# Kernel tuning notes

Measured on AMD Instinct MI355X. Metric: run time of the kernel, lower is better.

The kernel has to match this reference:

```python
import jax, jax.numpy as jnp
import numpy as np

B, S, D, H = 8, 1024, 768, 12
DK = D // H  # 64
EPS = 1e-8


def setup_inputs() -> dict:
    key = jax.random.key(0)
    ks = jax.random.split(key, 12)
    scale = 0.02
    inp = {
        "query": jax.random.normal(ks[0], (B, S, D), jnp.float32),
        "key": jax.random.normal(ks[1], (B, S, D), jnp.float32),
        "value": jax.random.normal(ks[2], (B, S, D), jnp.float32),
        "attention_mask": jnp.ones((B, 1, 1, S), jnp.float32),
        "Wq": jax.random.normal(ks[3], (D, D), jnp.float32) * scale,
        "bq": jnp.zeros((D,), jnp.float32),
        "Wk": jax.random.normal(ks[4], (D, D), jnp.float32) * scale,
        "bk": jnp.zeros((D,), jnp.float32),
        "Wv": jax.random.normal(ks[5], (D, D), jnp.float32) * scale,
        "bv": jnp.zeros((D,), jnp.float32),
        "Wo": jax.random.normal(ks[6], (D, D), jnp.float32) * scale,
        "bo": jnp.zeros((D,), jnp.float32),
        "gamma": jnp.ones((D,), jnp.float32),
        "beta": jnp.zeros((D,), jnp.float32),
    }
    return inp


def _split_heads(x):
    # [B,S,D] -> [B,H,S,DK]
    return x.reshape(B, S, H, DK).transpose(0, 2, 1, 3)


def reference(query, key, value, attention_mask, Wq, bq, Wk, bk, Wv, bv, Wo, bo, gamma, beta):
    origin = query
    q = _split_heads(query @ Wq + bq)
    k = _split_heads(key @ Wk + bk)
    v = _split_heads(value @ Wv + bv)
    # scaled dot-product attention, full [B,H,S,S] score as in original
    score = jnp.einsum('bhqd,bhkd->bhqk', q, k) / jnp.sqrt(jnp.float32(DK))
    score = score + (1.0 - attention_mask) * -10000.0
    attn = jax.nn.softmax(score, axis=-1)
    ctx = jnp.einsum('bhqk,bhkd->bhqd', attn, v)  # [B,H,S,DK]
    ctx = ctx.transpose(0, 2, 1, 3).reshape(B, S, D)
    out = ctx @ Wo + bo
    # residual + LayerNorm
    x = out + origin
    mu = jnp.mean(x, axis=-1, keepdims=True)
    var = jnp.mean(jnp.square(x - mu), axis=-1, keepdims=True)
    out = (x - mu) * jax.lax.rsqrt(var + EPS) * gamma + beta
    return out, attn
```

## Files before the change

### kernel.cpp

```cpp
#include <hip/hip_runtime.h>
#include <cstdint>

typedef unsigned short u16;
typedef __attribute__((ext_vector_type(8))) short bf16x8;
typedef __attribute__((ext_vector_type(4))) float f32x4;
typedef __attribute__((ext_vector_type(8))) unsigned short u16x8;

constexpr int NB = 8;
constexpr int SEQ = 1024;
constexpr int NH = 12;
constexpr int DM = 768;
constexpr int DH = 64;

__device__ __forceinline__ u16 f2bf(float f) {
  unsigned int x = __builtin_bit_cast(unsigned int, f);
  x += 0x7fffu + ((x >> 16) & 1u);
  return (u16)(x >> 16);
}

typedef __attribute__((address_space(1))) void* as1vp;
typedef __attribute__((address_space(3))) void* as3vp;

__device__ __forceinline__ void load_lds16(const u16* g, u16* l) {
  __builtin_amdgcn_global_load_lds((as1vp)(g), (as3vp)(l), 16, 0, 0);
}

template<int TM, int TN, int EPI>
__global__ __launch_bounds__(256)
void gemm_bt(const u16* __restrict__ A, int lda, long long strideA,
             const u16* __restrict__ BT, int ldb, long long strideBT,
             const float* __restrict__ bias,
             const float* __restrict__ extra,
             void* __restrict__ outp,
             int K)
{
  constexpr int BK = 32;
  constexpr int WM = TM / 2, WN = TN / 2;
  constexpr int FM = WM / 16, FN = WN / 16;
  __shared__ u16 As[TM * BK];
  __shared__ u16 Bs[TN * BK];
  const int tid = threadIdx.x;
  const int w = tid >> 6, l = tid & 63;
  const int z = blockIdx.z;
  const u16* Az = A + (long long)z * strideA;
  const u16* Bz = BT + (long long)z * strideBT;
  const int m0 = blockIdx.x * TM, n0 = blockIdx.y * TN;
  const int wm = (w & 1) * WM, wn = (w >> 1) * WN;
  const int quad = l >> 4, md = l & 15;

  f32x4 acc[FM][FN];
  f32x4 zero = {0.f, 0.f, 0.f, 0.f};
  #pragma unroll
  for (int i = 0; i < FM; ++i)
    #pragma unroll
    for (int j = 0; j < FN; ++j) acc[i][j] = zero;

  for (int k0 = 0; k0 < K; k0 += BK) {
    __syncthreads();
    #pragma unroll
    for (int r = 0; r < TM / 64; ++r) {
      int lin = r * 256 + tid;
      int row = lin >> 2, ch = lin & 3;
      load_lds16(Az + (long long)(m0 + row) * lda + k0 + ch * 8, &As[lin * 8]);
    }
    #pragma unroll
    for (int r = 0; r < TN / 64; ++r) {
      int lin = r * 256 + tid;
      int row = lin >> 2, ch = lin & 3;
      load_lds16(Bz + (long long)(n0 + row) * ldb + k0 + ch * 8, &Bs[lin * 8]);
    }
    __syncthreads();
    bf16x8 af[FM], bfr[FN];
    #pragma unroll
    for (int i = 0; i < FM; ++i)
      af[i] = *(const bf16x8*)&As[(wm + i * 16 + md) * BK + quad * 8];
    #pragma unroll
    for (int j = 0; j < FN; ++j)
      bfr[j] = *(const bf16x8*)&Bs[(wn + j * 16 + md) * BK + quad * 8];
    #pragma unroll
    for (int i = 0; i < FM; ++i)
      #pragma unroll
      for (int j = 0; j < FN; ++j)
        acc[i][j] = __builtin_amdgcn_mfma_f32_16x16x32_bf16(af[i], bfr[j], acc[i][j], 0, 0, 0);
  }

  #pragma unroll
  for (int i = 0; i < FM; ++i) {
    #pragma unroll
    for (int j = 0; j < FN; ++j) {
      #pragma unroll
      for (int r = 0; r < 4; ++r) {
        int grow = m0 + wm + i * 16 + quad * 4 + r;
        int gcol = n0 + wn + j * 16 + md;
        float v = acc[i][j][r];
        float vv = v + bias[gcol] + extra[(long long)grow * DM + gcol];
        ((float*)outp)[(long long)grow * DM + gcol] = vv;
      }
    }
  }
}

__global__ __launch_bounds__(256)
void gemm_qkv(const u16* __restrict__ Abase, const u16* __restrict__ Wbase,
              const float* __restrict__ bq, const float* __restrict__ bk,
              const float* __restrict__ bv, u16* __restrict__ outbase)
{
  constexpr int TM = 128, TN = 128, BK = 32;
  constexpr int WM = 64, WN = 64, FM = 4, FN = 4;
  __shared__ u16 As[TM * BK];
  __shared__ u16 Bs[TN * BK];
  const int tid = threadIdx.x;
  const int w = tid >> 6, l = tid & 63;
  const int z = blockIdx.z;
  const long long TOKDM = (long long)NB * SEQ * DM;
  const u16* Az = Abase + (long long)z * TOKDM;
  const u16* Bz = Wbase + (long long)z * DM * DM;
  const float* bias = z == 0 ? bq : z == 1 ? bk : bv;
  u16* o = outbase + (long long)z * TOKDM;
  const int m0 = blockIdx.x * TM, n0 = blockIdx.y * TN;
  const int wm = (w & 1) * WM, wn = (w >> 1) * WN;
  const int quad = l >> 4, md = l & 15;

  f32x4 acc[FM][FN];
  f32x4 zero = {0.f, 0.f, 0.f, 0.f};
  #pragma unroll
  for (int i = 0; i < FM; ++i)
    #pragma unroll
    for (int j = 0; j < FN; ++j) acc[i][j] = zero;

  for (int k0 = 0; k0 < DM; k0 += BK) {
    __syncthreads();
    #pragma unroll
    for (int r = 0; r < 2; ++r) {
      int lin = r * 256 + tid;
      int row = lin >> 2, ch = lin & 3;
      load_lds16(Az + (long long)(m0 + row) * DM + k0 + ch * 8, &As[lin * 8]);
    }
    #pragma unroll
    for (int r = 0; r < 2; ++r) {
      int lin = r * 256 + tid;
      int row = lin >> 2, ch = lin & 3;
      load_lds16(Bz + (long long)(n0 + row) * DM + k0 + ch * 8, &Bs[lin * 8]);
    }
    __syncthreads();
    bf16x8 af[FM], bfr[FN];
    #pragma unroll
    for (int i = 0; i < FM; ++i)
      af[i] = *(const bf16x8*)&As[(wm + i * 16 + md) * BK + quad * 8];
    #pragma unroll
    for (int j = 0; j < FN; ++j)
      bfr[j] = *(const bf16x8*)&Bs[(wn + j * 16 + md) * BK + quad * 8];
    #pragma unroll
    for (int i = 0; i < FM; ++i)
      #pragma unroll
      for (int j = 0; j < FN; ++j)
        acc[i][j] = __builtin_amdgcn_mfma_f32_16x16x32_bf16(af[i], bfr[j], acc[i][j], 0, 0, 0);
  }

  #pragma unroll
  for (int i = 0; i < FM; ++i) {
    #pragma unroll
    for (int j = 0; j < FN; ++j) {
      #pragma unroll
      for (int r = 0; r < 4; ++r) {
        int grow = m0 + wm + i * 16 + quad * 4 + r;
        int gcol = n0 + wn + j * 16 + md;
        int bb = grow >> 10, s = grow & (SEQ - 1);
        int h = gcol >> 6, dk = gcol & (DH - 1);
        float vb = acc[i][j][r] + bias[gcol];
        if (z < 2)
          o[(((long long)(bb * NH + h)) * SEQ + s) * DH + dk] = f2bf(vb);
        else
          o[(((long long)(bb * NH + h)) * DH + dk) * SEQ + s] = f2bf(vb);
      }
    }
  }
}

__global__ __launch_bounds__(256, 2)
void attn_fused(const u16* __restrict__ Qh, const u16* __restrict__ Kh,
                const u16* __restrict__ VT, const float* __restrict__ mask,
                float* __restrict__ attn, u16* __restrict__ ctx)
{
  __shared__ u16 Plds[4 * 32 * 128];
  const int tid = threadIdx.x;
  const int w = tid >> 6, l = tid & 63;
  const int quad = l >> 4, md = l & 15;
  const int dsp = blockIdx.x;
  const int L = (dsp & 7) * 96 + (dsp >> 3);
  const int bh = L >> 3, rb = L & 7;
  const int b = bh / NH, h = bh - b * NH;
  const int m0 = rb * 128;
  const int wm = w * 32;

  const u16* Qb = Qh + (long long)bh * SEQ * DH;
  const u16* Kb = Kh + (long long)bh * SEQ * DH;
  const u16* Vb = VT + (long long)bh * DH * SEQ;
  const float* mrow = mask + b * SEQ;
  float* arow = attn + (long long)bh * SEQ * SEQ;

  bf16x8 aq[2][2];
  #pragma unroll
  for (int i = 0; i < 2; ++i)
    #pragma unroll
    for (int kk = 0; kk < 2; ++kk)
      aq[i][kk] = *(const bf16x8*)(Qb + (long long)(m0 + wm + i * 16 + md) * DH + kk * 32 + quad * 8);

  float m_run[2][4], s_run[2][4];
  #pragma unroll
  for (int i = 0; i < 2; ++i)
    #pragma unroll
    for (int r = 0; r < 4; ++r) { m_run[i][r] = -3.0e38f; s_run[i][r] = 0.0f; }

  f32x4 zero = {0.f, 0.f, 0.f, 0.f};

  for (int t = 0; t < 8; ++t) {
    const int n0 = t * 128;
    float madd[8];
    #pragma unroll
    for (int j = 0; j < 8; ++j)
      madd[j] = (1.0f - mrow[n0 + j * 16 + md]) * -10000.0f;
    f32x4 acc[2][8];
    #pragma unroll
    for (int i = 0; i < 2; ++i)
      #pragma unroll
      for (int j = 0; j < 8; ++j) acc[i][j] = zero;
    #pragma unroll
    for (int j = 0; j < 8; ++j) {
      const u16* kp = Kb + (long long)(n0 + j * 16 + md) * DH + quad * 8;
      bf16x8 b0 = *(const bf16x8*)kp;
      bf16x8 b1 = *(const bf16x8*)(kp + 32);
      #pragma unroll
      for (int i = 0; i < 2; ++i) {
        acc[i][j] = __builtin_amdgcn_mfma_f32_16x16x32_bf16(aq[i][0], b0, acc[i][j], 0, 0, 0);
        acc[i][j] = __builtin_amdgcn_mfma_f32_16x16x32_bf16(aq[i][1], b1, acc[i][j], 0, 0, 0);
      }
    }
    #pragma unroll
    for (int i = 0; i < 2; ++i) {
      #pragma unroll
      for (int r = 0; r < 4; ++r) {
        float sc[8];
        float tm = -3.0e38f;
        #pragma unroll
        for (int j = 0; j < 8; ++j) {
          sc[j] = acc[i][j][r] * 0.125f + madd[j];
          tm = fmaxf(tm, sc[j]);
        }
        #pragma unroll
        for (int s = 1; s < 16; s <<= 1) tm = fmaxf(tm, __shfl_xor(tm, s, 64));
        float mn = fmaxf(m_run[i][r], tm);
        float ps = 0.0f;
        #pragma unroll
        for (int j = 0; j < 8; ++j) ps += __expf(sc[j] - mn);
        #pragma unroll
        for (int s = 1; s < 16; s <<= 1) ps += __shfl_xor(ps, s, 64);
        s_run[i][r] = s_run[i][r] * __expf(m_run[i][r] - mn) + ps;
        m_run[i][r] = mn;
      }
    }
  }
  float inv_s[2][4];
  #pragma unroll
  for (int i = 0; i < 2; ++i)
    #pragma unroll
    for (int r = 0; r < 4; ++r) inv_s[i][r] = 1.0f / s_run[i][r];

  f32x4 cacc[2][4];
  #pragma unroll
  for (int i = 0; i < 2; ++i)
    #pragma unroll
    for (int jd = 0; jd < 4; ++jd) cacc[i][jd] = zero;
  char* Pw = (char*)Plds + w * 8192;

  for (int t = 0; t < 8; ++t) {
    const int n0 = t * 128;
    float madd[8];
    #pragma unroll
    for (int j = 0; j < 8; ++j)
      madd[j] = (1.0f - mrow[n0 + j * 16 + md]) * -10000.0f;
    f32x4 acc[2][8];
    #pragma unroll
    for (int i = 0; i < 2; ++i)
      #pragma unroll
      for (int j = 0; j < 8; ++j) acc[i][j] = zero;
    #pragma unroll
    for (int j = 0; j < 8; ++j) {
      const u16* kp = Kb + (long long)(n0 + j * 16 + md) * DH + quad * 8;
      bf16x8 b0 = *(const bf16x8*)kp;
      bf16x8 b1 = *(const bf16x8*)(kp + 32);
      #pragma unroll
      for (int i = 0; i < 2; ++i) {
        acc[i][j] = __builtin_amdgcn_mfma_f32_16x16x32_bf16(aq[i][0], b0, acc[i][j], 0, 0, 0);
        acc[i][j] = __builtin_amdgcn_mfma_f32_16x16x32_bf16(aq[i][1], b1, acc[i][j], 0, 0, 0);
      }
    }
    #pragma unroll
    for (int i = 0; i < 2; ++i) {
      #pragma unroll
      for (int j = 0; j < 8; ++j) {
        #pragma unroll
        for (int r = 0; r < 4; ++r) {
          float p = __expf(acc[i][j][r] * 0.125f + madd[j] - m_run[i][r]) * inv_s[i][r];
          int grow = m0 + wm + i * 16 + quad * 4 + r;
          __builtin_nontemporal_store(p, &arow[(long long)grow * SEQ + n0 + j * 16 + md]);
          int rl = i * 16 + quad * 4 + r;
          int byo = (rl * 256 + (j * 16 + md) * 2) ^ ((rl & 7) << 4);
          *(u16*)(Pw + byo) = f2bf(p);
        }
      }
    }
    #pragma unroll
    for (int kk2 = 0; kk2 < 4; ++kk2) {
      bf16x8 ap[2];
      #pragma unroll
      for (int i = 0; i < 2; ++i) {
        int rl = i * 16 + md;
        int byo = (rl * 256 + (kk2 * 32 + quad * 8) * 2) ^ ((rl & 7) << 4);
        ap[i] = *(const bf16x8*)(Pw + byo);
      }
      #pragma unroll
      for (int jd = 0; jd < 4; ++jd) {
        bf16x8 bv = *(const bf16x8*)(Vb + (long long)(jd * 16 + md) * SEQ + n0 + kk2 * 32 + quad * 8);
        cacc[0][jd] = __builtin_amdgcn_mfma_f32_16x16x32_bf16(ap[0], bv, cacc[0][jd], 0, 0, 0);
        cacc[1][jd] = __builtin_amdgcn_mfma_f32_16x16x32_bf16(ap[1], bv, cacc[1][jd], 0, 0, 0);
      }
    }
  }

  #pragma unroll
  for (int i = 0; i < 2; ++i) {
    #pragma unroll
    for (int jd = 0; jd < 4; ++jd) {
      #pragma unroll
      for (int r = 0; r < 4; ++r) {
        int grow = m0 + wm + i * 16 + quad * 4 + r;
        ctx[((long long)(b * SEQ + grow)) * DM + h * DH + jd * 16 + md] = f2bf(cacc[i][jd][r]);
      }
    }
  }
}

__global__ __launch_bounds__(256) void layernorm_rows(const float* __restrict__ x,
    const float* __restrict__ gamma, const float* __restrict__ beta,
    float* __restrict__ out) {
  const int w = threadIdx.x >> 6, l = threadIdx.x & 63;
  const long long row = (long long)blockIdx.x * 4 + w;
  const float* px = x + row * DM;
  float v[12];
  float sum = 0.f;
  #pragma unroll
  for (int c = 0; c < 3; ++c) {
    float4 f = *(const float4*)&px[c * 256 + l * 4];
    v[c*4+0] = f.x; v[c*4+1] = f.y; v[c*4+2] = f.z; v[c*4+3] = f.w;
    sum += f.x + f.y + f.z + f.w;
  }
  #pragma unroll
  for (int s = 1; s < 64; s <<= 1) sum += __shfl_xor(sum, s, 64);
  float mu = sum * (1.0f / 768.0f);
  float s2 = 0.f;
  #pragma unroll
  for (int e = 0; e < 12; ++e) { float d = v[e] - mu; s2 += d * d; }
  #pragma unroll
  for (int s = 1; s < 64; s <<= 1) s2 += __shfl_xor(s2, s, 64);
  float rs = rsqrtf(s2 * (1.0f / 768.0f) + 1e-8f);
  #pragma unroll
  for (int c = 0; c < 3; ++c) {
    float4 o;
    #pragma unroll
    for (int e = 0; e < 4; ++e) {
      int col = c * 256 + l * 4 + e;
      ((float*)&o)[e] = (v[c*4+e] - mu) * rs * gamma[col] + beta[col];
    }
    *(float4*)&out[row * DM + c * 256 + l * 4] = o;
  }
}

__global__ __launch_bounds__(256) void castT_w(
    const float* __restrict__ W0, const float* __restrict__ W1,
    const float* __restrict__ W2, const float* __restrict__ W3,
    u16* __restrict__ Tbase) {
  __shared__ u16 t[64][65];
  const int z = blockIdx.z;
  const float* W = z == 0 ? W0 : z == 1 ? W1 : z == 2 ? W2 : W3;
  u16* T = Tbase + (long long)z * DM * DM;
  const int bx = blockIdx.x, by = blockIdx.y;
  #pragma unroll
  for (int it = 0; it < 16; ++it) {
    int idx = it * 256 + (int)threadIdx.x;
    int r = idx >> 6, c = idx & 63;
    t[r][c] = f2bf(W[(long long)(by * 64 + r) * DM + bx * 64 + c]);
  }
  __syncthreads();
  #pragma unroll
  for (int it = 0; it < 16; ++it) {
    int idx = it * 256 + (int)threadIdx.x;
    int r = idx >> 6, c = idx & 63;
    T[(long long)(bx * 64 + r) * DM + by * 64 + c] = t[c][r];
  }
}

__global__ __launch_bounds__(256) void cast3_bf16(
    const float* __restrict__ q, const float* __restrict__ k,
    const float* __restrict__ v, u16* __restrict__ dst) {
  const int z = blockIdx.z;
  const float* src = z == 0 ? q : z == 1 ? k : v;
  u16* d = dst + (long long)z * NB * SEQ * DM;
  long long i = ((long long)blockIdx.x * 256 + threadIdx.x) * 8;
  float4 f0 = *(const float4*)&src[i];
  float4 f1 = *(const float4*)&src[i + 4];
  u16x8 o;
  o[0] = f2bf(f0.x); o[1] = f2bf(f0.y); o[2] = f2bf(f0.z); o[3] = f2bf(f0.w);
  o[4] = f2bf(f1.x); o[5] = f2bf(f1.y); o[6] = f2bf(f1.z); o[7] = f2bf(f1.w);
  *(u16x8*)&d[i] = o;
}

extern "C" void kernel_launch(void* const* d_in, const int* in_sizes, int n_in,
                              void* d_out, int out_size, void* d_ws, size_t ws_size,
                              hipStream_t stream) {
  const float* query = (const float*)d_in[0];
  const float* key   = (const float*)d_in[1];
  const float* value = (const float*)d_in[2];
  const float* mask  = (const float*)d_in[3];
  const float* Wq = (const float*)d_in[4];
  const float* bq = (const float*)d_in[5];
  const float* Wk = (const float*)d_in[6];
  const float* bk = (const float*)d_in[7];
  const float* Wv = (const float*)d_in[8];
  const float* bv = (const float*)d_in[9];
  const float* Wo = (const float*)d_in[10];
  const float* bo = (const float*)d_in[11];
  const float* gamma = (const float*)d_in[12];
  const float* beta  = (const float*)d_in[13];

  const long long TOK = (long long)NB * SEQ;
  float* out  = (float*)d_out;
  float* attn = out + TOK * DM;

  u16* s0 = (u16*)d_ws;
  u16* s1 = s0 + TOK * DM;
  u16* s2 = s1 + TOK * DM;
  float* X = (float*)s1;

  u16* WqT = (u16*)d_out;
  u16* WoT = WqT + 3 * (long long)DM * DM;
  u16* ctx = WqT + 4 * (long long)DM * DM;
  u16* qB = (u16*)attn;

  castT_w<<<dim3(12, 12, 4), 256, 0, stream>>>(Wq, Wk, Wv, Wo, WqT);
  cast3_bf16<<<dim3(3072, 1, 3), 256, 0, stream>>>(query, key, value, qB);

  gemm_qkv<<<dim3(64, 6, 3), 256, 0, stream>>>(qB, WqT, bq, bk, bv, s0);

  attn_fused<<<dim3(768, 1, 1), 256, 0, stream>>>(s0, s1, s2, mask, attn, ctx);

  gemm_bt<128,128,4><<<dim3(64, 6, 1), 256, 0, stream>>>(
      ctx, DM, 0, WoT, DM, 0, bo, query, X, DM);

  layernorm_rows<<<(int)(TOK / 4), 256, 0, stream>>>(X, gamma, beta, out);
}
```

Baseline: 719.7 us.

## Shrink attention tile to 16 rows per wave, raise occupancy, use exp2

Each wave of the fused attention kernel now handles 16 query rows instead of 32, so a block covers 64 rows. This doubles the grid to 1536 blocks and halves the LDS tile, and launch bounds are raised to allow 4 blocks per CU. Softmax switches from __expf to exp2 with the log2(e) factor folded into the scale and mask constants. The attention-probability stores change from nontemporal to regular stores, and the LDS swizzle gains an extra XOR term. Smaller tiles mean K and V are re-read from global memory twice as often per query row, traded for lower register pressure and more latency hiding.

```diff
diff --git a/kernel.cpp b/kernel.cpp
--- a/kernel.cpp
+++ b/kernel.cpp
@@ -17,6 +17,12 @@
   x += 0x7fffu + ((x >> 16) & 1u);
   return (u16)(x >> 16);
 }
+
+#if __has_builtin(__builtin_amdgcn_exp2f)
+__device__ __forceinline__ float fexp2(float x) { return __builtin_amdgcn_exp2f(x); }
+#else
+__device__ __forceinline__ float fexp2(float x) { return exp2f(x); }
+#endif
 
 typedef __attribute__((address_space(1))) void* as1vp;
 typedef __attribute__((address_space(3))) void* as3vp;
@@ -177,21 +183,22 @@
   }
 }
 
-__global__ __launch_bounds__(256, 2)
+__global__ __launch_bounds__(256, 4)
 void attn_fused(const u16* __restrict__ Qh, const u16* __restrict__ Kh,
                 const u16* __restrict__ VT, const float* __restrict__ mask,
                 float* __restrict__ attn, u16* __restrict__ ctx)
 {
-  __shared__ u16 Plds[4 * 32 * 128];
+  __shared__ u16 Plds[4 * 16 * 128];
   const int tid = threadIdx.x;
   const int w = tid >> 6, l = tid & 63;
   const int quad = l >> 4, md = l & 15;
+  constexpr float SC2 = 0.125f * 1.4426950408889634f;
+  constexpr float MSK2 = -10000.0f * 1.4426950408889634f;
   const int dsp = blockIdx.x;
-  const int L = (dsp & 7) * 96 + (dsp >> 3);
-  const int bh = L >> 3, rb = L & 7;
+  const int L = (dsp & 7) * 192 + (dsp >> 3);
+  const int bh = L >> 4, rb = L & 15;
   const int b = bh / NH, h = bh - b * NH;
-  const int m0 = rb * 128;
-  const int wm = w * 32;
+  const int m0 = rb * 64 + w * 16;
 
   const u16* Qb = Qh + (long long)bh * SEQ * DH;
   const u16* Kb = Kh + (long long)bh * SEQ * DH;
@@ -199,144 +206,111 @@
   const float* mrow = mask + b * SEQ;
   float* arow = attn + (long long)bh * SEQ * SEQ;
 
-  bf16x8 aq[2][2];
-  #pragma unroll
-  for (int i = 0; i < 2; ++i)
-    #pragma unroll
-    for (int kk = 0; kk < 2; ++kk)
-      aq[i][kk] = *(const bf16x8*)(Qb + (long long)(m0 + wm + i * 16 + md) * DH + kk * 32 + quad * 8);
-
-  float m_run[2][4], s_run[2][4];
-  #pragma unroll
-  for (int i = 0; i < 2; ++i)
-    #pragma unroll
-    for (int r = 0; r < 4; ++r) { m_run[i][r] = -3.0e38f; s_run[i][r] = 0.0f; }
+  bf16x8 aq[2];
+  #pragma unroll
+  for (int kk = 0; kk < 2; ++kk)
+    aq[kk] = *(const bf16x8*)(Qb + (long long)(m0 + md) * DH + kk * 32 + quad * 8);
+
+  float m_run[4], s_run[4];
+  #pragma unroll
+  for (int r = 0; r < 4; ++r) { m_run[r] = -3.0e38f; s_run[r] = 0.0f; }
 
   f32x4 zero = {0.f, 0.f, 0.f, 0.f};
 
   for (int t = 0; t < 8; ++t) {
     const int n0 = t * 128;
-    float madd[8];
+    float madd2[8];
     #pragma unroll
     for (int j = 0; j < 8; ++j)
-      madd[j] = (1.0f - mrow[n0 + j * 16 + md]) * -10000.0f;
-    f32x4 acc[2][8];
-    #pragma unroll
-    for (int i = 0; i < 2; ++i)
-      #pragma unroll
-      for (int j = 0; j < 8; ++j) acc[i][j] = zero;
+      madd2[j] = (1.0f - mrow[n0 + j * 16 + md]) * MSK2;
+    f32x4 acc[8];
+    #pragma unroll
+    for (int j = 0; j < 8; ++j) acc[j] = zero;
     #pragma unroll
     for (int j = 0; j < 8; ++j) {
       const u16* kp = Kb + (long long)(n0 + j * 16 + md) * DH + quad * 8;
       bf16x8 b0 = *(const bf16x8*)kp;
       bf16x8 b1 = *(const bf16x8*)(kp + 32);
-      #pragma unroll
-      for (int i = 0; i < 2; ++i) {
-        acc[i][j] = __builtin_amdgcn_mfma_f32_16x16x32_bf16(aq[i][0], b0, acc[i][j], 0, 0, 0);
-        acc[i][j] = __builtin_amdgcn_mfma_f32_16x16x32_bf16(aq[i][1], b1, acc[i][j], 0, 0, 0);
+      acc[j] = __builtin_amdgcn_mfma_f32_16x16x32_bf16(aq[0], b0, acc[j], 0, 0, 0);
+      acc[j] = __builtin_amdgcn_mfma_f32_16x16x32_bf16(aq[1], b1, acc[j], 0, 0, 0);
+    }
+    #pragma unroll
+    for (int r = 0; r < 4; ++r) {
+      float sc[8];
+      float tm = -3.0e38f;
+      #pragma unroll
+      for (int j = 0; j < 8; ++j) {
+        sc[j] = acc[j][r] * SC2 + madd2[j];
+        tm = fmaxf(tm, sc[j]);
       }
-    }
-    #pragma unroll
-    for (int i = 0; i < 2; ++i) {
-      #pragma unroll
-      for (int r = 0; r < 4; ++r) {
-        float sc[8];
-        float tm = -3.0e38f;
-        #pragma unroll
-        for (int j = 0; j < 8; ++j) {
-          sc[j] = acc[i][j][r] * 0.125f + madd[j];
-          tm = fmaxf(tm, sc[j]);
-        }
-        #pragma unroll
-        for (int s = 1; s < 16; s <<= 1) tm = fmaxf(tm, __shfl_xor(tm, s, 64));
-        float mn = fmaxf(m_run[i][r], tm);
-        float ps = 0.0f;
-        #pragma unroll
-        for (int j = 0; j < 8; ++j) ps += __expf(sc[j] - mn);
-        #pragma unroll
-        for (int s = 1; s < 16; s <<= 1) ps += __shfl_xor(ps, s, 64);
-        s_run[i][r] = s_run[i][r] * __expf(m_run[i][r] - mn) + ps;
-        m_run[i][r] = mn;
-      }
-    }
-  }
-  float inv_s[2][4];
-  #pragma unroll
-  for (int i = 0; i < 2; ++i)
-    #pragma unroll
-    for (int r = 0; r < 4; ++r) inv_s[i][r] = 1.0f / s_run[i][r];
-
-  f32x4 cacc[2][4];
-  #pragma unroll
-  for (int i = 0; i < 2; ++i)
-    #pragma unroll
-    for (int jd = 0; jd < 4; ++jd) cacc[i][jd] = zero;
-  char* Pw = (char*)Plds + w * 8192;
+      #pragma unroll
+      for (int s = 1; s < 16; s <<= 1) tm = fmaxf(tm, __shfl_xor(tm, s, 64));
+      float mn = fmaxf(m_run[r], tm);
+      float ps = 0.0f;
+      #pragma unroll
+      for (int j = 0; j < 8; ++j) ps += fexp2(sc[j] - mn);
+      #pragma unroll
+      for (int s = 1; s < 16; s <<= 1) ps += __shfl_xor(ps, s, 64);
+      s_run[r] = s_run[r] * fexp2(m_run[r] - mn) + ps;
+      m_run[r] = mn;
+    }
+  }
+  float inv_s[4];
+  #pragma unroll
+  for (int r = 0; r < 4; ++r) inv_s[r] = 1.0f / s_run[r];
+
+  f32x4 cacc[4];
+  #pragma unroll
+  for (int jd = 0; jd < 4; ++jd) cacc[jd] = zero;
+  char* Pw = (char*)Plds + w * 4096;
 
   for (int t = 0; t < 8; ++t) {
     const int n0 = t * 128;
-    float madd[8];
+    float madd2[8];
     #pragma unroll
     for (int j = 0; j < 8; ++j)
-      madd[j] = (1.0f - mrow[n0 + j * 16 + md]) * -10000.0f;
-    f32x4 acc[2][8];
-    #pragma unroll
-    for (int i = 0; i < 2; ++i)
-      #pragma unroll
-      for (int j = 0; j < 8; ++j) acc[i][j] = zero;
+      madd2[j] = (1.0f - mrow[n0 + j * 16 + md]) * MSK2;
+    f32x4 acc[8];
+    #pragma unroll
+    for (int j = 0; j < 8; ++j) acc[j] = zero;
     #pragma unroll
     for (int j = 0; j < 8; ++j) {
       const u16* kp = Kb + (long long)(n0 + j * 16 + md) * DH + quad * 8;
       bf16x8 b0 = *(const bf16x8*)kp;
       bf16x8 b1 = *(const bf16x8*)(kp + 32);
-      #pragma unroll
-      for (int i = 0; i < 2; ++i) {
-        acc[i][j] = __builtin_amdgcn_mfma_f32_16x16x32_bf16(aq[i][0], b0, acc[i][j], 0, 0, 0);
-        acc[i][j] = __builtin_amdgcn_mfma_f32_16x16x32_bf16(aq[i][1], b1, acc[i][j], 0, 0, 0);
+      acc[j] = __builtin_amdgcn_mfma_f32_16x16x32_bf16(aq[0], b0, acc[j], 0, 0, 0);
+      acc[j] = __builtin_amdgcn_mfma_f32_16x16x32_bf16(aq[1], b1, acc[j], 0, 0, 0);
+    }
+    #pragma unroll
+    for (int j = 0; j < 8; ++j) {
+      #pragma unroll
+      for (int r = 0; r < 4; ++r) {
+        float p = fexp2(acc[j][r] * SC2 + madd2[j] - m_run[r]) * inv_s[r];
+        int grow = m0 + quad * 4 + r;
+        arow[(long long)grow * SEQ + n0 + j * 16 + md] = p;
+        int rl = quad * 4 + r;
+        int byo = (rl * 256 + (j * 16 + md) * 2) ^ ((rl & 7) << 4) ^ ((rl & 8) << 2);
+        *(u16*)(Pw + byo) = f2bf(p);
       }
     }
     #pragma unroll
-    for (int i = 0; i < 2; ++i) {
-      #pragma unroll
-      for (int j = 0; j < 8; ++j) {
-        #pragma unroll
-        for (int r = 0; r < 4; ++r) {
-          float p = __expf(acc[i][j][r] * 0.125f + madd[j] - m_run[i][r]) * inv_s[i][r];
-          int grow = m0 + wm + i * 16 + quad * 4 + r;
-          __builtin_nontemporal_store(p, &arow[(long long)grow * SEQ + n0 + j * 16 + md]);
-          int rl = i * 16 + quad * 4 + r;
-          int byo = (rl * 256 + (j * 16 + md) * 2) ^ ((rl & 7) << 4);
-          *(u16*)(Pw + byo) = f2bf(p);
-        }
-      }
-    }
-    #pragma unroll
     for (int kk2 = 0; kk2 < 4; ++kk2) {
-      bf16x8 ap[2];
-      #pragma unroll
-      for (int i = 0; i < 2; ++i) {
-        int rl = i * 16 + md;
-        int byo = (rl * 256 + (kk2 * 32 + quad * 8) * 2) ^ ((rl & 7) << 4);
-        ap[i] = *(const bf16x8*)(Pw + byo);
-      }
+      int byo = (md * 256 + (kk2 * 32 + quad * 8) * 2) ^ ((md & 7) << 4) ^ ((md & 8) << 2);
+      bf16x8 ap = *(const bf16x8*)(Pw + byo);
       #pragma unroll
       for (int jd = 0; jd < 4; ++jd) {
         bf16x8 bv = *(const bf16x8*)(Vb + (long long)(jd * 16 + md) * SEQ + n0 + kk2 * 32 + quad * 8);
-        cacc[0][jd] = __builtin_amdgcn_mfma_f32_16x16x32_bf16(ap[0], bv, cacc[0][jd], 0, 0, 0);
-        cacc[1][jd] = __builtin_amdgcn_mfma_f32_16x16x32_bf16(ap[1], bv, cacc[1][jd], 0, 0, 0);
+        cacc[jd] = __builtin_amdgcn_mfma_f32_16x16x32_bf16(ap, bv, cacc[jd], 0, 0, 0);
       }
     }
   }
 
   #pragma unroll
-  for (int i = 0; i < 2; ++i) {
-    #pragma unroll
-    for (int jd = 0; jd < 4; ++jd) {
-      #pragma unroll
-      for (int r = 0; r < 4; ++r) {
-        int grow = m0 + wm + i * 16 + quad * 4 + r;
-        ctx[((long long)(b * SEQ + grow)) * DM + h * DH + jd * 16 + md] = f2bf(cacc[i][jd][r]);
-      }
+  for (int jd = 0; jd < 4; ++jd) {
+    #pragma unroll
+    for (int r = 0; r < 4; ++r) {
+      int grow = m0 + quad * 4 + r;
+      ctx[((long long)(b * SEQ + grow)) * DM + h * DH + jd * 16 + md] = f2bf(cacc[jd][r]);
     }
   }
 }
@@ -452,7 +426,7 @@
 
   gemm_qkv<<<dim3(64, 6, 3), 256, 0, stream>>>(qB, WqT, bq, bk, bv, s0);
 
-  attn_fused<<<dim3(768, 1, 1), 256, 0, stream>>>(s0, s1, s2, mask, attn, ctx);
+  attn_fused<<<dim3(1536, 1, 1), 256, 0, stream>>>(s0, s1, s2, mask, attn, ctx);
 
   gemm_bt<128,128,4><<<dim3(64, 6, 1), 256, 0, stream>>>(
       ctx, DM, 0, WoT, DM, 0, bo, query, X, DM);
```

Result: slower. 1.009 ms (+40.2%).

## Stage attention probabilities through LDS for vectorized coalesced stores, use exp2

Applied to the files above, without the earlier changes.

Attention probabilities are now written to global memory by reading back the per-wave bf16 tile in LDS and issuing 16-byte nontemporal stores per lane along rows, replacing scattered 4-byte stores. This targets poorly coalesced writes of the large attention matrix. The LDS swizzle gets an extra bit, and softmax switches to exp2 with constants pre-scaled by log2(e). As a tradeoff, the stored probabilities are now rounded to bf16 precision.

```diff
diff --git a/kernel.cpp b/kernel.cpp
--- a/kernel.cpp
+++ b/kernel.cpp
@@ -17,6 +17,16 @@
   x += 0x7fffu + ((x >> 16) & 1u);
   return (u16)(x >> 16);
 }
+
+__device__ __forceinline__ float bf2f(u16 u) {
+  return __builtin_bit_cast(float, (unsigned int)u << 16);
+}
+
+#if __has_builtin(__builtin_amdgcn_exp2f)
+__device__ __forceinline__ float fexp2(float x) { return __builtin_amdgcn_exp2f(x); }
+#else
+__device__ __forceinline__ float fexp2(float x) { return exp2f(x); }
+#endif
 
 typedef __attribute__((address_space(1))) void* as1vp;
 typedef __attribute__((address_space(3))) void* as3vp;
@@ -186,6 +196,8 @@
   const int tid = threadIdx.x;
   const int w = tid >> 6, l = tid & 63;
   const int quad = l >> 4, md = l & 15;
+  constexpr float SC2 = 0.125f * 1.4426950408889634f;
+  constexpr float MSK2 = -10000.0f * 1.4426950408889634f;
   const int dsp = blockIdx.x;
   const int L = (dsp & 7) * 96 + (dsp >> 3);
   const int bh = L >> 3, rb = L & 7;
@@ -216,10 +228,10 @@
 
   for (int t = 0; t < 8; ++t) {
     const int n0 = t * 128;
-    float madd[8];
+    float madd2[8];
     #pragma unroll
     for (int j = 0; j < 8; ++j)
-      madd[j] = (1.0f - mrow[n0 + j * 16 + md]) * -10000.0f;
+      madd2[j] = (1.0f - mrow[n0 + j * 16 + md]) * MSK2;
     f32x4 acc[2][8];
     #pragma unroll
     for (int i = 0; i < 2; ++i)
@@ -244,7 +256,7 @@
         float tm = -3.0e38f;
         #pragma unroll
         for (int j = 0; j < 8; ++j) {
-          sc[j] = acc[i][j][r] * 0.125f + madd[j];
+          sc[j] = acc[i][j][r] * SC2 + madd2[j];
           tm = fmaxf(tm, sc[j]);
         }
         #pragma unroll
@@ -252,10 +264,10 @@
         float mn = fmaxf(m_run[i][r], tm);
         float ps = 0.0f;
         #pragma unroll
-        for (int j = 0; j < 8; ++j) ps += __expf(sc[j] - mn);
+        for (int j = 0; j < 8; ++j) ps += fexp2(sc[j] - mn);
         #pragma unroll
         for (int s = 1; s < 16; s <<= 1) ps += __shfl_xor(ps, s, 64);
-        s_run[i][r] = s_run[i][r] * __expf(m_run[i][r] - mn) + ps;
+        s_run[i][r] = s_run[i][r] * fexp2(m_run[i][r] - mn) + ps;
         m_run[i][r] = mn;
       }
     }
@@ -272,13 +284,15 @@
     #pragma unroll
     for (int jd = 0; jd < 4; ++jd) cacc[i][jd] = zero;
   char* Pw = (char*)Plds + w * 8192;
+  const int srl = l >> 1, sch = l & 1;
+  float* gp0 = arow + (long long)(m0 + wm + srl) * SEQ + sch * 64;
 
   for (int t = 0; t < 8; ++t) {
     const int n0 = t * 128;
-    float madd[8];
+    float madd2[8];
     #pragma unroll
     for (int j = 0; j < 8; ++j)
-      madd[j] = (1.0f - mrow[n0 + j * 16 + md]) * -10000.0f;
+      madd2[j] = (1.0f - mrow[n0 + j * 16 + md]) * MSK2;
     f32x4 acc[2][8];
     #pragma unroll
     for (int i = 0; i < 2; ++i)
@@ -301,22 +315,35 @@
       for (int j = 0; j < 8; ++j) {
         #pragma unroll
         for (int r = 0; r < 4; ++r) {
-          float p = __expf(acc[i][j][r] * 0.125f + madd[j] - m_run[i][r]) * inv_s[i][r];
-          int grow = m0 + wm + i * 16 + quad * 4 + r;
-          __builtin_nontemporal_store(p, &arow[(long long)grow * SEQ + n0 + j * 16 + md]);
+          float p = fexp2(acc[i][j][r] * SC2 + madd2[j] - m_run[i][r]) * inv_s[i][r];
           int rl = i * 16 + quad * 4 + r;
-          int byo = (rl * 256 + (j * 16 + md) * 2) ^ ((rl & 7) << 4);
+          int byo = (rl * 256 + (j * 16 + md) * 2) ^ ((rl & 7) << 4) ^ ((rl & 8) << 2);
           *(u16*)(Pw + byo) = f2bf(p);
         }
       }
     }
+    {
+      float* gp = gp0 + n0;
+      #pragma unroll
+      for (int g = 0; g < 8; ++g) {
+        int byo = (srl * 256 + (sch * 64 + g * 8) * 2) ^ ((srl & 7) << 4) ^ ((srl & 8) << 2);
+        u16x8 pk = *(const u16x8*)(Pw + byo);
+        f32x4 o0, o1;
+        #pragma unroll
+        for (int e = 0; e < 4; ++e) o0[e] = bf2f(pk[e]);
+        #pragma unroll
+        for (int e = 0; e < 4; ++e) o1[e] = bf2f(pk[4 + e]);
+        __builtin_nontemporal_store(o0, (f32x4*)(gp + g * 8));
+        __builtin_nontemporal_store(o1, (f32x4*)(gp + g * 8 + 4));
+      }
+    }
     #pragma unroll
     for (int kk2 = 0; kk2 < 4; ++kk2) {
       bf16x8 ap[2];
       #pragma unroll
       for (int i = 0; i < 2; ++i) {
         int rl = i * 16 + md;
-        int byo = (rl * 256 + (kk2 * 32 + quad * 8) * 2) ^ ((rl & 7) << 4);
+        int byo = (rl * 256 + (kk2 * 32 + quad * 8) * 2) ^ ((rl & 7) << 4) ^ ((rl & 8) << 2);
         ap[i] = *(const bf16x8*)(Pw + byo);
       }
       #pragma unroll
```

New measurement: 1.641 ms. 2.28x slower.
